# Kernel optimization log

Hardware: AMD Instinct MI355X
Metric: run time of the kernel (lower is better)

Reference implementation:

```python
import jax, jax.numpy as jnp
import numpy as np

# Static problem sizes (uniform graphs for jit-friendliness)
B = 64          # number of hypergraphs in the batch
N_PER = 32      # shape-nodes per hypergraph (num_nodes_hgraph, uniform)
D_ID = 256      # shape_id_dim
D_MULT = 64     # shape_multiplicity_dim
LATENT = 512    # latent_dim
D_NODE = D_ID + D_MULT           # 320
FEAT = 3 * D_NODE + LATENT       # 1472, MLP input dim
HID = 2 * FEAT                   # 2944
NUM_ATOMS = 11                   # 1 + feature_sizes['num_atoms']
VOCAB_ID, VOCAB_MULT = 100, 20


def setup_inputs() -> dict:
    key = jax.random.key(0)
    ks = jax.random.split(key, 11)
    s1 = 1.0 / np.sqrt(FEAT)
    s2 = 1.0 / np.sqrt(HID)
    s3 = 1.0 / np.sqrt(FEAT)
    return {
        "shape_node_idx": jax.random.randint(ks[0], (B * N_PER,), 0, VOCAB_ID),
        "shape_node_mult": jax.random.randint(ks[1], (B * N_PER,), 0, VOCAB_MULT),
        "z_graph": jax.random.normal(ks[2], (B, LATENT), jnp.float32),
        "id_emb": jax.random.normal(ks[3], (VOCAB_ID, D_ID), jnp.float32) * 0.02,
        "mult_emb": jax.random.normal(ks[4], (VOCAB_MULT, D_MULT), jnp.float32) * 0.02,
        "W1": jax.random.normal(ks[5], (FEAT, HID), jnp.float32) * s1,
        "b1": jnp.zeros((HID,), jnp.float32),
        "W2": jax.random.normal(ks[6], (HID, FEAT), jnp.float32) * s2,
        "b2": jnp.zeros((FEAT,), jnp.float32),
        "W3": jax.random.normal(ks[7], (FEAT, NUM_ATOMS), jnp.float32) * s3,
        "b3": jnp.zeros((NUM_ATOMS,), jnp.float32),
    }


def reference(shape_node_idx, shape_node_mult, z_graph, id_emb, mult_emb,
              W1, b1, W2, b2, W3, b3):
    # Node features: concat of shape-id and multiplicity embeddings -> [B, n, d_node]
    x = jnp.concatenate([id_emb[shape_node_idx], mult_emb[shape_node_mult]], axis=-1)
    x = x.reshape(B, N_PER, D_NODE)

    # Per-graph segment aggregation (node_aggregation='mean') -> [B, d_node]
    agg = x.mean(axis=1)

    # All intra-graph node pairs (block-diagonal edge pattern), edge (i, j):
    # input = [x_i, x_j, z_graph, agg] broadcast to [B, n, n, FEAT]
    xi = jnp.broadcast_to(x[:, :, None, :], (B, N_PER, N_PER, D_NODE))
    xj = jnp.broadcast_to(x[:, None, :, :], (B, N_PER, N_PER, D_NODE))
    zg = jnp.broadcast_to(z_graph[:, None, None, :], (B, N_PER, N_PER, LATENT))
    ag = jnp.broadcast_to(agg[:, None, None, :], (B, N_PER, N_PER, D_NODE))
    feat = jnp.concatenate([xi, xj, zg, ag], axis=-1)  # [B, n, n, FEAT]

    # MLP [FEAT, 2*FEAT, FEAT, NUM_ATOMS] with ReLU activations
    h = jax.nn.relu(jnp.einsum('bijf,fh->bijh', feat, W1) + b1)
    h = jax.nn.relu(jnp.einsum('bijh,hf->bijf', h, W2) + b2)
    logits = jnp.einsum('bijf,fa->bija', h, W3) + b3  # [B, n, n, A]

    # _to_symmetric: average each edge value with its transpose
    logits = 0.5 * (logits + jnp.swapaxes(logits, 1, 2))

    # Flattened per-edge logits (matches sparse COO value order: row-major pairs)
    return logits.reshape(B * N_PER * N_PER, NUM_ATOMS)
```

## Files before the change

kernel.cpp:

```cpp
#include <hip/hip_runtime.h>
#include <stdint.h>

#define NBG   64
#define NPER  32
#define DNODE 320
#define FEAT  1472
#define HIDN  2944
#define FEATP 1536
#define NA    11
#define NROWS 2048
#define MEDGE 65536

typedef __attribute__((ext_vector_type(8))) short    bf16x8;
typedef __attribute__((ext_vector_type(4))) float    fv4;
typedef __attribute__((ext_vector_type(4))) unsigned uiv4;

__device__ __forceinline__ unsigned short f2bf(float f) {
  unsigned u = __builtin_bit_cast(unsigned, f);
  u += 0x7fffu + ((u >> 16) & 1u);
  return (unsigned short)(u >> 16);
}
__device__ __forceinline__ float bf2f(unsigned short h) {
  unsigned u = ((unsigned)h) << 16;
  return __builtin_bit_cast(float, u);
}
__device__ __forceinline__ unsigned cvt_pk_bf16(float lo, float hi) {
  unsigned r;
  asm("v_cvt_pk_bf16_f32 %0, %1, %2" : "=v"(r) : "v"(lo), "v"(hi));
  return r;
}
__device__ __forceinline__ void gload_lds16(const void* g, void* l) {
  __builtin_amdgcn_global_load_lds((const __attribute__((address_space(1))) void*)g,
                                   (__attribute__((address_space(3))) void*)l, 16, 0, 0);
}

__global__ void k_transpose_bf16(const float* __restrict__ src, unsigned short* __restrict__ dst,
                                 int K, int N, int Npad) {
  __shared__ float tile[64][65];
  int k0 = blockIdx.x * 64, n0 = blockIdx.y * 64;
  int r = threadIdx.x >> 2, cb = (threadIdx.x & 3) * 16;
  const float* srow = src + (size_t)(k0 + r) * N + n0 + cb;
#pragma unroll
  for (int c = 0; c < 16; ++c) {
    int n = n0 + cb + c;
    tile[r][cb + c] = (n < N) ? srow[c] : 0.f;
  }
  __syncthreads();
  unsigned short* drow = dst + (size_t)(n0 + r) * K + k0 + cb;
#pragma unroll
  for (int c = 0; c < 16; ++c) drow[c] = f2bf(tile[cb + c][r]);
}

__global__ void k_embed(const int* __restrict__ idx, const int* __restrict__ mlt,
                        const float* __restrict__ id_emb, const float* __restrict__ mult_emb,
                        unsigned short* __restrict__ xb) {
  int t = blockIdx.x, c = threadIdx.x;
  int iv = idx[t], mv = mlt[t];
  xb[t * DNODE + c] = f2bf(id_emb[iv * 256 + c]);
  if (c < 64) xb[t * DNODE + 256 + c] = f2bf(mult_emb[mv * 64 + c]);
}

__global__ void k_agg(const unsigned short* __restrict__ xb, float* __restrict__ agg) {
  int b = blockIdx.x;
  for (int d = threadIdx.x; d < DNODE; d += 256) {
    float s = 0.f;
    for (int i = 0; i < NPER; ++i) s += bf2f(xb[(b * NPER + i) * DNODE + d]);
    agg[b * DNODE + d] = s * (1.f / 32.f);
  }
}

__global__ void k_za(const float* __restrict__ z, const float* __restrict__ agg,
                     unsigned short* __restrict__ za) {
  int b = blockIdx.x;
  for (int c = threadIdx.x; c < 832; c += 256) {
    unsigned short v = 0;
    if (b < NBG) v = (c < 512) ? f2bf(z[b * 512 + c]) : f2bf(agg[b * DNODE + (c - 512)]);
    za[b * 832 + c] = v;
  }
}

__global__ void k_gemm1(const unsigned short* __restrict__ A, int sA, int Mrows,
                        const unsigned short* __restrict__ W1T, int kOff, int Ksteps,
                        float* __restrict__ C, const float* __restrict__ bias) {
  __shared__ alignas(16) unsigned short Als[128 * 32];
  __shared__ alignas(16) unsigned short Bls[128 * 32];
  int bx = blockIdx.x;
  int mt = bx / 23, nc = bx - mt * 23;
  int m0 = mt * 128, n0 = nc * 128;
  int tid = threadIdx.x, lane = tid & 63, w = tid >> 6;

  fv4 acc[4][4] = {};
  for (int kt = 0; kt < Ksteps; ++kt) {
    int k0 = kt * 32;
    __syncthreads();
#pragma unroll
    for (int q = 0; q < 2; ++q) {
      int seg = w * 2 + q;
      int row = seg * 16 + (lane >> 2);
      int col = (lane & 3) * 8;
      gload_lds16(A + (size_t)(m0 + row) * sA + k0 + col, &Als[seg * 512]);
      gload_lds16(W1T + (size_t)(n0 + row) * FEAT + kOff + k0 + col, &Bls[seg * 512]);
    }
    __syncthreads();
    bf16x8 aF[4], bF[4];
#pragma unroll
    for (int mf = 0; mf < 4; ++mf)
      aF[mf] = *(const bf16x8*)&Als[((w >> 1) * 64 + mf * 16 + (lane & 15)) * 32 + (lane >> 4) * 8];
#pragma unroll
    for (int nf = 0; nf < 4; ++nf)
      bF[nf] = *(const bf16x8*)&Bls[((w & 1) * 64 + nf * 16 + (lane & 15)) * 32 + (lane >> 4) * 8];
#pragma unroll
    for (int mf = 0; mf < 4; ++mf)
#pragma unroll
      for (int nf = 0; nf < 4; ++nf)
        acc[mf][nf] = __builtin_amdgcn_mfma_f32_16x16x32_bf16(aF[mf], bF[nf], acc[mf][nf], 0, 0, 0);
  }
  int mq = (w >> 1) * 64, nq = (w & 1) * 64;
#pragma unroll
  for (int mf = 0; mf < 4; ++mf)
#pragma unroll
    for (int nf = 0; nf < 4; ++nf) {
      int n = n0 + nq + nf * 16 + (lane & 15);
      float bv = bias ? bias[n] : 0.f;
#pragma unroll
      for (int r = 0; r < 4; ++r) {
        int m = m0 + mq + mf * 16 + (lane >> 4) * 4 + r;
        if (m < Mrows) C[(size_t)m * HIDN + n] = acc[mf][nf][r] + bv;
      }
    }
}

__global__ void k_pq(float* __restrict__ P1, const float* __restrict__ Q) {
  int r = blockIdx.x;
  const float* q = Q + (size_t)(r >> 5) * HIDN;
  float* p = P1 + (size_t)r * HIDN;
  for (int n = threadIdx.x; n < HIDN; n += 256) p[n] += q[n];
}

__global__ __launch_bounds__(256, 2)
void k_gemm2(const float* __restrict__ PQ1, const float* __restrict__ P2,
             const unsigned short* __restrict__ W2T,
             const float* __restrict__ b2, const float* __restrict__ W3,
             float* __restrict__ Lraw) {
  __shared__ alignas(16) unsigned char LB[54272];
  int raw = blockIdx.x;
  int mt = (raw & 7) * 64 + (raw >> 3);
  int m0 = mt * 128;
  int tid = threadIdx.x, lane = tid & 63, w = tid >> 6;
  int bG = m0 >> 10;
  int i0 = (m0 >> 5) & 31;
  int ks = lane >> 4;
  int r  = lane & 15;
  int il0 = (w >> 1) * 2;

  const int swcolB = ((lane & 3) ^ ((lane >> 3) & 3)) * 8;
  const int swcolP = (((lane >> 1) & 3) ^ ((lane >> 3) & 3)) * 8 + (lane & 1) * 4;

  float* wred = (float*)(LB + 43008);
  for (int e = tid; e < 4 * 704; e += 256) wred[e] = 0.f;

  auto STAGEB = [&](int nc, int kt, int buf) {
#pragma unroll
    for (int q = 0; q < 4; ++q) {
      int seg = w * 4 + q;
      int row = seg * 16 + (lane >> 2);
      gload_lds16(W2T + (size_t)(nc * 256 + row) * HIDN + kt * 32 + swcolB,
                  LB + buf * 16384 + seg * 1024);
    }
  };
  auto STAGESRC = [&](int kt, int buf) {
    gload_lds16(P2 + (size_t)(bG * NPER + 8 * w + (lane >> 3)) * HIDN + kt * 32 + swcolP,
                LB + 32768 + buf * 4096 + w * 1024);
    if (w == 0)
      gload_lds16(PQ1 + (size_t)(bG * NPER + i0 + (lane >> 3)) * HIDN + kt * 32 + (lane & 7) * 4,
                  LB + 40960 + buf * 1024);
  };

  fv4 acc[4][8] = {};

  STAGEB(0, 0, 0);
  STAGESRC(0, 0);
  __syncthreads();

  int nc_c = 0, kt_c = 0;
  for (int s = 0; s < 552; ++s) {
    int cur = s & 1;
    if (s < 551) {
      int kt_s = kt_c + 1, nc_s = nc_c;
      if (kt_s == 92) { kt_s = 0; ++nc_s; }
      STAGEB(nc_s, kt_s, cur ^ 1);
      STAGESRC(kt_s, cur ^ 1);
    }

    const unsigned char* Bb = LB + cur * 16384;
    const unsigned char* Pb = LB + 32768 + cur * 4096;
    const unsigned char* Qb = LB + 40960 + cur * 1024;

    int psw = (ks ^ (r & 3)) * 32;
    fv4 q0[2], q1[2], p0[2], p1[2];
#pragma unroll
    for (int h = 0; h < 2; ++h) {
      q0[h] = *(const fv4*)(Qb + il0 * 128 + ks * 32 + h * 16);
      q1[h] = *(const fv4*)(Qb + (il0 + 1) * 128 + ks * 32 + h * 16);
      p0[h] = *(const fv4*)(Pb + r * 128 + psw + h * 16);
      p1[h] = *(const fv4*)(Pb + (16 + r) * 128 + psw + h * 16);
    }
    bf16x8 bF[8];
#pragma unroll
    for (int nf = 0; nf < 8; ++nf) {
      int brow = (w & 1) * 128 + nf * 16 + r;
      int slot = ks ^ ((brow >> 1) & 3);
      bF[nf] = *(const bf16x8*)(Bb + brow * 64 + slot * 16);
    }

    bf16x8 aF[4];
#pragma unroll
    for (int mf = 0; mf < 4; ++mf) {
      fv4 s0 = (mf & 2 ? q1[0] : q0[0]) + (mf & 1 ? p1[0] : p0[0]);
      fv4 s1 = (mf & 2 ? q1[1] : q0[1]) + (mf & 1 ? p1[1] : p0[1]);
      uiv4 u;
      u[0] = cvt_pk_bf16(fmaxf(s0[0], 0.f), fmaxf(s0[1], 0.f));
      u[1] = cvt_pk_bf16(fmaxf(s0[2], 0.f), fmaxf(s0[3], 0.f));
      u[2] = cvt_pk_bf16(fmaxf(s1[0], 0.f), fmaxf(s1[1], 0.f));
      u[3] = cvt_pk_bf16(fmaxf(s1[2], 0.f), fmaxf(s1[3], 0.f));
      aF[mf] = __builtin_bit_cast(bf16x8, u);
    }

#pragma unroll
    for (int nf = 0; nf < 8; ++nf)
#pragma unroll
      for (int mf = 0; mf < 4; ++mf)
        acc[mf][nf] = __builtin_amdgcn_mfma_f32_16x16x32_bf16(aF[mf], bF[nf], acc[mf][nf], 0, 0, 0);

    if (kt_c == 91) {
      int nq = (w & 1) * 128;
#pragma unroll
      for (int mf = 0; mf < 4; ++mf) {
        float sv[4][NA];
#pragma unroll
        for (int rr = 0; rr < 4; ++rr)
#pragma unroll
          for (int a = 0; a < NA; ++a) sv[rr][a] = 0.f;
#pragma unroll
        for (int nf = 0; nf < 8; ++nf) {
          int n = nc_c * 256 + nq + nf * 16 + r;
          if (n < FEAT) {
            float bv = b2[n];
            float w3r[NA];
#pragma unroll
            for (int a = 0; a < NA; ++a) w3r[a] = W3[n * NA + a];
#pragma unroll
            for (int rr = 0; rr < 4; ++rr) {
              float h = fmaxf(acc[mf][nf][rr] + bv, 0.f);
#pragma unroll
              for (int a = 0; a < NA; ++a) sv[rr][a] += h * w3r[a];
            }
          }
        }
#pragma unroll
        for (int off = 1; off < 16; off <<= 1)
#pragma unroll
          for (int rr = 0; rr < 4; ++rr)
#pragma unroll
            for (int a = 0; a < NA; ++a) sv[rr][a] += __shfl_xor(sv[rr][a], off, 64);
        int a = r;
        if (a < NA) {
#pragma unroll
          for (int rr = 0; rr < 4; ++rr)
            wred[w * 704 + (mf * 16 + ks * 4 + rr) * NA + a] += sv[rr][a];
        }
      }
#pragma unroll
      for (int mf = 0; mf < 4; ++mf)
#pragma unroll
        for (int nf = 0; nf < 8; ++nf)
          acc[mf][nf] = fv4{0.f, 0.f, 0.f, 0.f};
    }
    __syncthreads();
    if (++kt_c == 92) { kt_c = 0; ++nc_c; }
  }

  for (int e = tid; e < 128 * NA; e += 256) {
    int row = e / NA, a = e - row * NA;
    int wr = row >> 6, rr = row & 63;
    float v = wred[(wr * 2 + 0) * 704 + rr * NA + a] + wred[(wr * 2 + 1) * 704 + rr * NA + a];
    Lraw[(size_t)(m0 + row) * NA + a] = v;
  }
}

__global__ void k_sym(const float* __restrict__ Lraw, const float* __restrict__ b3,
                      float* __restrict__ out) {
  int e = blockIdx.x * 256 + threadIdx.x;
  if (e >= MEDGE * NA) return;
  int m = e / NA, a = e - m * NA;
  int msw = (m & ~1023) | ((m & 31) << 5) | ((m >> 5) & 31);
  out[e] = 0.5f * (Lraw[e] + Lraw[(size_t)msw * NA + a]) + b3[a];
}

extern "C" void kernel_launch(void* const* d_in, const int* in_sizes, int n_in,
                              void* d_out, int out_size, void* d_ws, size_t ws_size,
                              hipStream_t stream) {
  const int*   idx      = (const int*)d_in[0];
  const int*   mlt      = (const int*)d_in[1];
  const float* z        = (const float*)d_in[2];
  const float* id_emb   = (const float*)d_in[3];
  const float* mult_emb = (const float*)d_in[4];
  const float* W1       = (const float*)d_in[5];
  const float* b1       = (const float*)d_in[6];
  const float* W2       = (const float*)d_in[7];
  const float* b2       = (const float*)d_in[8];
  const float* W3       = (const float*)d_in[9];
  const float* b3       = (const float*)d_in[10];
  float* out = (float*)d_out;

  uint8_t* ws = (uint8_t*)d_ws;
  size_t o = 0;
  auto alloc = [&](size_t bytes) { size_t r = o; o += (bytes + 255) & ~(size_t)255; return r; };
  size_t oW1T = alloc((size_t)HIDN * FEAT * 2);
  size_t oW2T = alloc((size_t)FEATP * HIDN * 2);
  size_t oXB  = alloc((size_t)NROWS * DNODE * 2);
  size_t oZA  = alloc((size_t)128 * 832 * 2);
  size_t oAG  = alloc((size_t)NBG * DNODE * 4);
  size_t oP1  = alloc((size_t)NROWS * HIDN * 4);
  size_t oP2  = alloc((size_t)NROWS * HIDN * 4);
  size_t oQ   = alloc((size_t)NBG * HIDN * 4);
  size_t oLR  = alloc((size_t)MEDGE * NA * 4);
  if (ws_size < o) return;

  unsigned short* W1T = (unsigned short*)(ws + oW1T);
  unsigned short* W2T = (unsigned short*)(ws + oW2T);
  unsigned short* xb  = (unsigned short*)(ws + oXB);
  unsigned short* za  = (unsigned short*)(ws + oZA);
  float* agg = (float*)(ws + oAG);
  float* P1  = (float*)(ws + oP1);
  float* P2  = (float*)(ws + oP2);
  float* Qm  = (float*)(ws + oQ);
  float* LR  = (float*)(ws + oLR);

  k_transpose_bf16<<<dim3(FEAT / 64, HIDN / 64), 256, 0, stream>>>(W1, W1T, FEAT, HIDN, HIDN);
  k_transpose_bf16<<<dim3(HIDN / 64, FEATP / 64), 256, 0, stream>>>(W2, W2T, HIDN, FEAT, FEATP);
  k_embed<<<NROWS, 256, 0, stream>>>(idx, mlt, id_emb, mult_emb, xb);
  k_agg<<<NBG, 256, 0, stream>>>(xb, agg);
  k_za<<<128, 256, 0, stream>>>(z, agg, za);
  k_gemm1<<<16 * 23, 256, 0, stream>>>(xb, DNODE, NROWS, W1T, 0, 10, P1, nullptr);
  k_gemm1<<<16 * 23, 256, 0, stream>>>(xb, DNODE, NROWS, W1T, 320, 10, P2, nullptr);
  k_gemm1<<<1 * 23, 256, 0, stream>>>(za, 832, NBG, W1T, 640, 26, Qm, b1);
  k_pq<<<NROWS, 256, 0, stream>>>(P1, Qm);
  k_gemm2<<<512, 256, 0, stream>>>(P1, P2, W2T, b2, W3, LR);
  k_sym<<<(MEDGE * NA + 255) / 256, 256, 0, stream>>>(LR, b3, out);
}
```

Measured before the change: 1.176 ms.

## Prefetch two stages ahead with vmcnt-gated barriers and MFMA priority boost

Restructures the double-buffered main loop so global-to-LDS loads run two iterations ahead instead of one. Each wave waits with a partial vmcnt for only its older batch of loads, then hits a raw s_barrier instead of __syncthreads. The MFMA block is also wrapped in s_setprio to favor matrix issue. The goal is to hide global load latency behind compute, at the cost of hand-counted vmcnt values that must match the exact number of loads issued per wave.

```diff
diff --git a/kernel.cpp b/kernel.cpp
--- a/kernel.cpp
+++ b/kernel.cpp
@@ -175,22 +175,25 @@
       gload_lds16(PQ1 + (size_t)(bG * NPER + i0 + (lane >> 3)) * HIDN + kt * 32 + (lane & 7) * 4,
                   LB + 40960 + buf * 1024);
   };
+#define GATE_BATCH()                                                        \
+  do {                                                                      \
+    if (w == 0) asm volatile("s_waitcnt vmcnt(6)" ::: "memory");            \
+    else        asm volatile("s_waitcnt vmcnt(5)" ::: "memory");            \
+  } while (0)
 
   fv4 acc[4][8] = {};
 
   STAGEB(0, 0, 0);
   STAGESRC(0, 0);
-  __syncthreads();
+  STAGEB(0, 1, 1);
+  STAGESRC(1, 1);
+  GATE_BATCH();
+  __builtin_amdgcn_s_barrier();
+  __builtin_amdgcn_sched_barrier(0);
 
   int nc_c = 0, kt_c = 0;
   for (int s = 0; s < 552; ++s) {
     int cur = s & 1;
-    if (s < 551) {
-      int kt_s = kt_c + 1, nc_s = nc_c;
-      if (kt_s == 92) { kt_s = 0; ++nc_s; }
-      STAGEB(nc_s, kt_s, cur ^ 1);
-      STAGESRC(kt_s, cur ^ 1);
-    }
 
     const unsigned char* Bb = LB + cur * 16384;
     const unsigned char* Pb = LB + 32768 + cur * 4096;
@@ -226,11 +229,13 @@
       aF[mf] = __builtin_bit_cast(bf16x8, u);
     }
 
+    __builtin_amdgcn_s_setprio(1);
 #pragma unroll
     for (int nf = 0; nf < 8; ++nf)
 #pragma unroll
       for (int mf = 0; mf < 4; ++mf)
         acc[mf][nf] = __builtin_amdgcn_mfma_f32_16x16x32_bf16(aF[mf], bF[nf], acc[mf][nf], 0, 0, 0);
+    __builtin_amdgcn_s_setprio(0);
 
     if (kt_c == 91) {
       int nq = (w & 1) * 128;
@@ -276,16 +281,34 @@
         for (int nf = 0; nf < 8; ++nf)
           acc[mf][nf] = fv4{0.f, 0.f, 0.f, 0.f};
     }
-    __syncthreads();
+
+    asm volatile("s_waitcnt lgkmcnt(0)" ::: "memory");
+    __builtin_amdgcn_s_barrier();
+    __builtin_amdgcn_sched_barrier(0);
+
+    if (s + 2 < 552) {
+      int kt2 = kt_c + 2, nc2 = nc_c;
+      if (kt2 >= 92) { kt2 -= 92; ++nc2; }
+      STAGEB(nc2, kt2, cur);
+      STAGESRC(kt2, cur);
+      GATE_BATCH();
+    } else if (s + 1 < 552) {
+      asm volatile("s_waitcnt vmcnt(0)" ::: "memory");
+    }
+    __builtin_amdgcn_s_barrier();
+    __builtin_amdgcn_sched_barrier(0);
+
     if (++kt_c == 92) { kt_c = 0; ++nc_c; }
   }
 
+  __syncthreads();
   for (int e = tid; e < 128 * NA; e += 256) {
     int row = e / NA, a = e - row * NA;
     int wr = row >> 6, rr = row & 63;
     float v = wred[(wr * 2 + 0) * 704 + rr * NA + a] + wred[(wr * 2 + 1) * 704 + rr * NA + a];
     Lraw[(size_t)(m0 + row) * NA + a] = v;
   }
+#undef GATE_BATCH
 }
 
 __global__ void k_sym(const float* __restrict__ Lraw, const float* __restrict__ b3,
```

Result: no change. 1.196 ms (+1.7%).
